# Optimization experiments

Measured on AMD Instinct MI355X. Metric: run time of the kernel, lower is better.

Reference implementation:

```python
import jax, jax.numpy as jnp
import numpy as np

EMBED = 256      # hp.embed_size
ATT = 256        # hp.attention_size
KSZ = 5          # hp.kernel_size
L = 4            # hp.decoder_layers
N_MELS = 80
R = 4
KEY_PR = (4096 // 4) / 512.0   # hp.max_frames // hp.r / hp.max_timesteps = 2.0
QUERY_PR = 1.0
SQRT_HALF = float(np.sqrt(0.5))


def _pos_enc(T, C, pos_rate):
    # Faithful to source: angle_rates = pos*pos_rate/10000^(2*(k//2)/C); pe = pos*angle_rates
    pos = jnp.arange(T, dtype=jnp.float32)[:, None]            # [T,1]
    k = jnp.arange(C)[None, :]                                  # [1,C]
    power = jnp.power(jnp.float32(10000.0), 2.0 * (k // 2).astype(jnp.float32) / C)
    angle = pos * (pos * pos_rate / power)                      # [T,C]
    return jnp.where(k % 2 == 0, jnp.sin(angle), jnp.cos(angle))[None]  # [1,T,C]


def _conv_block(x, w, b, dilation):
    # causal dilated Conv1D + GLU + scaled residual. x:[B,T,C], w:[K,C,2C]
    pad = (KSZ - 1) * dilation
    y = jax.lax.conv_general_dilated(
        x, w, window_strides=(1,), padding=[(pad, 0)], rhs_dilation=(dilation,),
        dimension_numbers=('NWC', 'WIO', 'NWC')) + b
    a, g = jnp.split(y, 2, axis=-1)
    return (x + a * jax.nn.sigmoid(g)) * SQRT_HALF


def _attention(x, keys, values, w1, b1, w2, b2, w3, b3, wo, bo):
    Tq, Tk, C = x.shape[1], keys.shape[1], x.shape[-1]
    q = x + _pos_enc(Tq, C, QUERY_PR)
    k = keys + _pos_enc(Tk, C, KEY_PR)
    k_out = k @ w1 + b1           # fc1(keys)
    q_out = q @ w2 + b2           # fc2(query)
    v_out = values @ w3 + b3      # fc3(values)
    aw = jnp.einsum('bqd,bkd->bqk', q_out, k_out)
    # key_masks = ones_like(sum(keys_out,-1)) -> never zero, masking is a no-op (kept faithful)
    al = jax.nn.softmax(aw, axis=-1)  # dropout disabled (training=False)
    ctx = jnp.einsum('bqk,bkd->bqd', al, v_out) * jax.lax.rsqrt(jnp.float32(Tk))
    return ctx @ wo + bo


def setup_inputs() -> dict:
    key = jax.random.key(0)
    ks = jax.random.split(key, 16)
    s = jnp.float32(0.02)
    B, TQ, TK = 32, 1024, 512
    d = {}
    d['inputs'] = jax.random.normal(ks[0], (B, TQ, N_MELS * R), jnp.float32)
    d['keys'] = jax.random.normal(ks[1], (B, TK, EMBED), jnp.float32)
    d['values'] = jax.random.normal(ks[2], (B, TK, EMBED), jnp.float32)
    d['w_first'] = jax.random.normal(ks[3], (N_MELS * R, EMBED), jnp.float32) * s
    d['b_first'] = jnp.zeros((EMBED,), jnp.float32)
    d['fc_w'] = jax.random.normal(ks[4], (L - 1, EMBED, EMBED), jnp.float32) * s
    d['fc_b'] = jnp.zeros((L - 1, EMBED), jnp.float32)
    d['conv_w'] = jax.random.normal(ks[5], (L, KSZ, EMBED, 2 * EMBED), jnp.float32) * s
    d['conv_b'] = jnp.zeros((L, 2 * EMBED), jnp.float32)
    d['att_w1'] = jax.random.normal(ks[6], (L, EMBED, ATT), jnp.float32) * s
    d['att_b1'] = jnp.zeros((L, ATT), jnp.float32)
    d['att_w2'] = jax.random.normal(ks[7], (L, EMBED, ATT), jnp.float32) * s
    d['att_b2'] = jnp.zeros((L, ATT), jnp.float32)
    d['att_w3'] = jax.random.normal(ks[8], (L, EMBED, ATT), jnp.float32) * s
    d['att_b3'] = jnp.zeros((L, ATT), jnp.float32)
    d['att_wo'] = jax.random.normal(ks[9], (L, ATT, EMBED), jnp.float32) * s
    d['att_bo'] = jnp.zeros((L, EMBED), jnp.float32)
    d['w_done'] = jax.random.normal(ks[10], (EMBED, 2), jnp.float32) * s
    d['b_done'] = jnp.zeros((2,), jnp.float32)
    d['w_mel'] = jax.random.normal(ks[11], (EMBED, N_MELS * R), jnp.float32) * s
    d['b_mel'] = jnp.zeros((N_MELS * R,), jnp.float32)
    return d


def reference(inputs, keys, values, w_first, b_first, fc_w, fc_b, conv_w, conv_b,
              att_w1, att_b1, att_w2, att_b2, att_w3, att_b3, att_wo, att_bo,
              w_done, b_done, w_mel, b_mel):
    h = jax.nn.relu(inputs @ w_first + b_first)
    for i in range(L - 1):
        h = jax.nn.relu(h @ fc_w[i] + fc_b[i])
    for i in range(L):
        h = _conv_block(h, conv_w[i], conv_b[i], 2 ** i)
        att = _attention(h, keys, values,
                         att_w1[i], att_b1[i], att_w2[i], att_b2[i],
                         att_w3[i], att_b3[i], att_wo[i], att_bo[i])
        h = (att + h) * SQRT_HALF
    done_output = jax.nn.sigmoid(h @ w_done + b_done)
    mel_output = h @ w_mel + b_mel
    return (mel_output, done_output, h)
```

## Files before the change

kernel.cpp:

```cpp
#include <hip/hip_runtime.h>
#include <hip/hip_bf16.h>
#include <math.h>

#define SQH 0.70710678118654752440f

typedef __bf16 bf16x8 __attribute__((ext_vector_type(8)));
typedef float f32x4 __attribute__((ext_vector_type(4)));

__device__ __forceinline__ void glds16(const void* g, void* l) {
    __builtin_amdgcn_global_load_lds((const __attribute__((address_space(1))) void*)g,
                                     (__attribute__((address_space(3))) void*)l, 16, 0, 0);
}

__device__ __forceinline__ int xcd_swz(int lin, int n) {
    if (n & 7) return lin;
    return (lin & 7) * (n >> 3) + (lin >> 3);
}

__global__ void pos_enc_kernel(float* __restrict__ pe, int T, float rate) {
    int idx = blockIdx.x * blockDim.x + threadIdx.x;
    if (idx >= T * 256) return;
    int t = idx >> 8;
    int k = idx & 255;
    float e = 2.0f * (float)(k >> 1) / 256.0f;
    float pw = powf(10000.0f, e);
    float ang = (float)t * ((float)t * rate / pw);
    pe[idx] = ((k & 1) == 0) ? sinf(ang) : cosf(ang);
}

__global__ void zero_init(float* z) { z[threadIdx.x] = 0.f; }

__global__ __launch_bounds__(256) void cvt_bf(const float* __restrict__ src,
                                              __bf16* __restrict__ dst, long n8) {
    long i = (long)blockIdx.x * 256 + threadIdx.x;
    if (i >= n8) return;
    const float* s = src + i * 8;
    float4 a = *(const float4*)s, b = *(const float4*)(s + 4);
    bf16x8 o;
    o[0] = (__bf16)a.x; o[1] = (__bf16)a.y; o[2] = (__bf16)a.z; o[3] = (__bf16)a.w;
    o[4] = (__bf16)b.x; o[5] = (__bf16)b.y; o[6] = (__bf16)b.z; o[7] = (__bf16)b.w;
    *(bf16x8*)(dst + i * 8) = o;
}

__global__ __launch_bounds__(256) void kpe_kernel(const float* __restrict__ keys,
                                                  const float* __restrict__ pek,
                                                  __bf16* __restrict__ dst) {
    long i = (long)blockIdx.x * 256 + threadIdx.x;
    long row = i >> 5; int c8 = (int)(i & 31) << 3;
    const float* kp = keys + row * 256 + c8;
    const float* pp = pek + (row & 511) * 256 + c8;
    float4 a = *(const float4*)kp, b = *(const float4*)(kp + 4);
    float4 p = *(const float4*)pp, q = *(const float4*)(pp + 4);
    bf16x8 o;
    o[0] = (__bf16)(a.x + p.x); o[1] = (__bf16)(a.y + p.y);
    o[2] = (__bf16)(a.z + p.z); o[3] = (__bf16)(a.w + p.w);
    o[4] = (__bf16)(b.x + q.x); o[5] = (__bf16)(b.y + q.y);
    o[6] = (__bf16)(b.z + q.z); o[7] = (__bf16)(b.w + q.w);
    *(bf16x8*)(dst + i * 8) = o;
}

__global__ __launch_bounds__(256) void transpose_k(const float* __restrict__ src,
                                                   __bf16* __restrict__ dst,
                                                   int R, int Cc, long sS, long sD) {
    __shared__ float tile[32][33];
    src += (long)blockIdx.z * sS;
    dst += (long)blockIdx.z * sD;
    int c0 = blockIdx.x * 32, r0 = blockIdx.y * 32;
    int tx = threadIdx.x & 31, ty = threadIdx.x >> 5;
#pragma unroll
    for (int p = 0; p < 4; ++p)
        tile[ty + 8 * p][tx] = src[(long)(r0 + ty + 8 * p) * Cc + c0 + tx];
    __syncthreads();
#pragma unroll
    for (int p = 0; p < 4; ++p)
        dst[(long)(c0 + ty + 8 * p) * R + r0 + tx] = (__bf16)tile[tx][ty + 8 * p];
}

template<int BIAS_MODE, int ACT, int OUT_MODE, int RES>
__global__ __launch_bounds__(256) void gemm_bf(
    const __bf16* __restrict__ A, const __bf16* __restrict__ Bt,
    const float* __restrict__ bias, const float* __restrict__ res,
    float* __restrict__ outF, __bf16* __restrict__ outB,
    int M, int N, int K, long sA, long sB, long sC)
{
    __shared__ __align__(16) __bf16 As[4096];
    __shared__ __align__(16) __bf16 Bs[4096];
    const int gx = gridDim.x, gy = gridDim.y;
    int lin = (blockIdx.z * gy + blockIdx.y) * gx + blockIdx.x;
    lin = xcd_swz(lin, gx * gy * gridDim.z);
    const int bx = lin % gx, by = (lin / gx) % gy, z = lin / (gx * gy);
    A += (long)z * sA;
    Bt += (long)z * sB;
    const int row0 = by << 7, col0 = bx << 7;
    const int tid = threadIdx.x, wid = tid >> 6, lane = tid & 63;
    const int lrow = lane & 15, lkp = lane >> 4;
    const int wm = (wid >> 1) << 6, wn = (wid & 1) << 6;
    const int srow = (wid << 5) + (lane >> 2);
    const int kq8 = (lane & 3) << 3;
    const __bf16* Ap0 = A + (long)(row0 + srow) * K + kq8;
    const __bf16* Ap1 = Ap0 + (long)16 * K;
    int c0i = col0 + srow, c1i = col0 + srow + 16;
    if (c0i > N - 1) c0i = N - 1;
    if (c1i > N - 1) c1i = N - 1;
    const __bf16* Bp0 = Bt + (long)c0i * K + kq8;
    const __bf16* Bp1 = Bt + (long)c1i * K + kq8;
    __bf16* AsW = As + (wid << 10);
    __bf16* BsW = Bs + (wid << 10);

    f32x4 acc[4][4];
#pragma unroll
    for (int i = 0; i < 4; ++i)
#pragma unroll
        for (int j = 0; j < 4; ++j) acc[i][j] = (f32x4){0.f, 0.f, 0.f, 0.f};

    for (int k0 = 0; k0 < K; k0 += 32) {
        glds16(Ap0 + k0, AsW);
        glds16(Ap1 + k0, AsW + 512);
        glds16(Bp0 + k0, BsW);
        glds16(Bp1 + k0, BsW + 512);
        __syncthreads();
        bf16x8 af[4], bfr[4];
        const __bf16* Ar = As + (wm + lrow) * 32 + lkp * 8;
        const __bf16* Br = Bs + (wn + lrow) * 32 + lkp * 8;
#pragma unroll
        for (int i = 0; i < 4; ++i) af[i] = *(const bf16x8*)(Ar + i * 512);
#pragma unroll
        for (int j = 0; j < 4; ++j) bfr[j] = *(const bf16x8*)(Br + j * 512);
#pragma unroll
        for (int i = 0; i < 4; ++i)
#pragma unroll
            for (int j = 0; j < 4; ++j)
                acc[i][j] = __builtin_amdgcn_mfma_f32_16x16x32_bf16(af[i], bfr[j], acc[i][j], 0, 0, 0);
        __syncthreads();
    }

    float* oF = outF ? outF + (long)z * sC : nullptr;
    __bf16* oB = outB ? outB + (long)z * sC : nullptr;
    const float* resp = RES ? res + (long)z * sC : nullptr;
#pragma unroll
    for (int i = 0; i < 4; ++i) {
#pragma unroll
        for (int r = 0; r < 4; ++r) {
            const int gr = row0 + wm + i * 16 + lkp * 4 + r;
#pragma unroll
            for (int j = 0; j < 4; ++j) {
                const int gc = col0 + wn + j * 16 + lrow;
                if (gc >= N) continue;
                float v = acc[i][j][r];
                if (BIAS_MODE == 1) v += bias[gc];
                if (BIAS_MODE == 2) v += bias[gr];
                if (RES) v = (v + resp[(long)gr * N + gc]) * SQH;
                if (ACT == 1) v = fmaxf(v, 0.f);
                if (OUT_MODE == 0 || OUT_MODE == 2) oF[(long)gr * N + gc] = v;
                if (OUT_MODE == 1 || OUT_MODE == 2) oB[(long)gr * N + gc] = (__bf16)v;
            }
        }
    }
}

__global__ __launch_bounds__(256) void conv_glu(
    const __bf16* __restrict__ hbf, const float* __restrict__ hin,
    const __bf16* __restrict__ Wt, const float* __restrict__ bias,
    const float* __restrict__ peq,
    float* __restrict__ hc_f, __bf16* __restrict__ hc_b, __bf16* __restrict__ hq_b,
    int dil, const __bf16* __restrict__ zp)
{
    __shared__ __align__(16) __bf16 As[4096];
    __shared__ __align__(16) __bf16 Ba[4096];
    __shared__ __align__(16) __bf16 Bg[4096];
    const int gx = gridDim.x;
    int lin = blockIdx.y * gx + blockIdx.x;
    lin = xcd_swz(lin, gx * gridDim.y);
    const int bx = lin % gx, by = lin / gx;
    const int row0 = by << 7, col0 = bx << 7;
    const int tid = threadIdx.x, wid = tid >> 6, lane = tid & 63;
    const int lrow = lane & 15, lkp = lane >> 4;
    const int wm = (wid >> 1) << 6, wn = (wid & 1) << 6;
    const int srow = (wid << 5) + (lane >> 2);
    const int kq8 = (lane & 3) << 3;
    const int grow = row0 + srow;
    const int t0 = (row0 & 1023) + srow;
    const __bf16* Ba0 = Wt + (long)(col0 + srow) * 1280 + kq8;
    const __bf16* Ba1 = Ba0 + (long)16 * 1280;
    const __bf16* Bg0 = Wt + (long)(col0 + 256 + srow) * 1280 + kq8;
    const __bf16* Bg1 = Bg0 + (long)16 * 1280;
    __bf16* AsW = As + (wid << 10);
    __bf16* BaW = Ba + (wid << 10);
    __bf16* BgW = Bg + (wid << 10);

    f32x4 aca[4][4], acg[4][4];
#pragma unroll
    for (int i = 0; i < 4; ++i)
#pragma unroll
        for (int j = 0; j < 4; ++j) {
            aca[i][j] = (f32x4){0.f, 0.f, 0.f, 0.f};
            acg[i][j] = (f32x4){0.f, 0.f, 0.f, 0.f};
        }

    for (int k0 = 0; k0 < 1280; k0 += 32) {
        const int tap = k0 >> 8;
        const int off = (4 - tap) * dil;
        const int kc = (k0 & 255) + kq8;
        const __bf16* a0 = (t0 >= off) ? hbf + (long)(grow - off) * 256 + kc : zp;
        const __bf16* a1 = (t0 + 16 >= off) ? hbf + (long)(grow + 16 - off) * 256 + kc : zp;
        glds16(a0, AsW);
        glds16(a1, AsW + 512);
        glds16(Ba0 + k0, BaW);
        glds16(Ba1 + k0, BaW + 512);
        glds16(Bg0 + k0, BgW);
        glds16(Bg1 + k0, BgW + 512);
        __syncthreads();
        bf16x8 af[4], ba[4], bg[4];
        const __bf16* Ar = As + (wm + lrow) * 32 + lkp * 8;
        const __bf16* Bar = Ba + (wn + lrow) * 32 + lkp * 8;
        const __bf16* Bgr = Bg + (wn + lrow) * 32 + lkp * 8;
#pragma unroll
        for (int i = 0; i < 4; ++i) af[i] = *(const bf16x8*)(Ar + i * 512);
#pragma unroll
        for (int j = 0; j < 4; ++j) { ba[j] = *(const bf16x8*)(Bar + j * 512); bg[j] = *(const bf16x8*)(Bgr + j * 512); }
#pragma unroll
        for (int i = 0; i < 4; ++i)
#pragma unroll
            for (int j = 0; j < 4; ++j) {
                aca[i][j] = __builtin_amdgcn_mfma_f32_16x16x32_bf16(af[i], ba[j], aca[i][j], 0, 0, 0);
                acg[i][j] = __builtin_amdgcn_mfma_f32_16x16x32_bf16(af[i], bg[j], acg[i][j], 0, 0, 0);
            }
        __syncthreads();
    }
#pragma unroll
    for (int i = 0; i < 4; ++i) {
#pragma unroll
        for (int r = 0; r < 4; ++r) {
            const int gr = row0 + wm + i * 16 + lkp * 4 + r;
            const long rb = (long)gr * 256;
            const long pb = (long)(gr & 1023) * 256;
#pragma unroll
            for (int j = 0; j < 4; ++j) {
                const int ca = col0 + wn + j * 16 + lrow;
                float a = aca[i][j][r] + bias[ca];
                float g = acg[i][j][r] + bias[ca + 256];
                float v = (hin[rb + ca] + a / (1.f + expf(-g))) * SQH;
                hc_f[rb + ca] = v;
                hc_b[rb + ca] = (__bf16)v;
                hq_b[rb + ca] = (__bf16)(v + peq[pb + ca]);
            }
        }
    }
}

__global__ __launch_bounds__(512) void scores_sm(
    const __bf16* __restrict__ Q, const __bf16* __restrict__ Kb,
    __bf16* __restrict__ aw)
{
    __shared__ __align__(16) __bf16 As[128 * 32];
    __shared__ __align__(16) __bf16 Bs[512 * 32];
    __shared__ float redM[4][128];
    __shared__ float redS[4][128];
    int lin = xcd_swz(blockIdx.x, gridDim.x);
    const int rt = lin & 7, z = lin >> 3;
    const int row0 = rt << 7;
    const __bf16* Az = Q + (long)z * 1024 * 256;
    const __bf16* Bz = Kb + (long)z * 512 * 256;
    __bf16* awz = aw + (long)z * 1024 * 512;
    const int tid = threadIdx.x, wid = tid >> 6, lane = tid & 63;
    const int lrow = lane & 15, lkp = lane >> 4;
    const int wr = wid >> 2, wc = wid & 3;
    const int sr = lane >> 2;
    const int kq8 = (lane & 3) << 3;

    f32x4 acc[4][8];
#pragma unroll
    for (int i = 0; i < 4; ++i)
#pragma unroll
        for (int j = 0; j < 8; ++j) acc[i][j] = (f32x4){0.f, 0.f, 0.f, 0.f};

    for (int k0 = 0; k0 < 256; k0 += 32) {
        glds16(Az + (long)(row0 + (wid << 4) + sr) * 256 + k0 + kq8, As + (wid << 9));
#pragma unroll
        for (int c = 0; c < 4; ++c) {
            const int R = ((c << 3) + wid) << 4;
            glds16(Bz + (long)(R + sr) * 256 + k0 + kq8, Bs + (R << 5));
        }
        __syncthreads();
        bf16x8 af[4], bfr[8];
        const __bf16* Ar = As + ((wr << 6) + lrow) * 32 + lkp * 8;
        const __bf16* Br = Bs + ((wc << 7) + lrow) * 32 + lkp * 8;
#pragma unroll
        for (int i = 0; i < 4; ++i) af[i] = *(const bf16x8*)(Ar + i * 512);
#pragma unroll
        for (int j = 0; j < 8; ++j) bfr[j] = *(const bf16x8*)(Br + j * 512);
#pragma unroll
        for (int i = 0; i < 4; ++i)
#pragma unroll
            for (int j = 0; j < 8; ++j)
                acc[i][j] = __builtin_amdgcn_mfma_f32_16x16x32_bf16(af[i], bfr[j], acc[i][j], 0, 0, 0);
        __syncthreads();
    }

    float mx[4][4];
#pragma unroll
    for (int i = 0; i < 4; ++i)
#pragma unroll
        for (int r = 0; r < 4; ++r) {
            float m = acc[i][0][r];
#pragma unroll
            for (int j = 1; j < 8; ++j) m = fmaxf(m, acc[i][j][r]);
#pragma unroll
            for (int s = 1; s < 16; s <<= 1) m = fmaxf(m, __shfl_xor(m, s));
            mx[i][r] = m;
        }
    if (lrow == 0) {
#pragma unroll
        for (int i = 0; i < 4; ++i)
#pragma unroll
            for (int r = 0; r < 4; ++r)
                redM[wc][(wr << 6) + i * 16 + (lkp << 2) + r] = mx[i][r];
    }
    __syncthreads();
    float sm[4][4];
#pragma unroll
    for (int i = 0; i < 4; ++i)
#pragma unroll
        for (int r = 0; r < 4; ++r) {
            const int row = (wr << 6) + i * 16 + (lkp << 2) + r;
            float m = fmaxf(fmaxf(redM[0][row], redM[1][row]), fmaxf(redM[2][row], redM[3][row]));
            float s = 0.f;
#pragma unroll
            for (int j = 0; j < 8; ++j) {
                float p = expf(acc[i][j][r] - m);
                acc[i][j][r] = p;
                s += p;
            }
#pragma unroll
            for (int sft = 1; sft < 16; sft <<= 1) s += __shfl_xor(s, sft);
            sm[i][r] = s;
        }
    if (lrow == 0) {
#pragma unroll
        for (int i = 0; i < 4; ++i)
#pragma unroll
            for (int r = 0; r < 4; ++r)
                redS[wc][(wr << 6) + i * 16 + (lkp << 2) + r] = sm[i][r];
    }
    __syncthreads();
#pragma unroll
    for (int i = 0; i < 4; ++i)
#pragma unroll
        for (int r = 0; r < 4; ++r) {
            const int row = (wr << 6) + i * 16 + (lkp << 2) + r;
            float S = redS[0][row] + redS[1][row] + redS[2][row] + redS[3][row];
            float sc = 0.04419417382415922f / S;
            __bf16* op = awz + (long)(row0 + row) * 512 + (wc << 7) + lrow;
#pragma unroll
            for (int j = 0; j < 8; ++j)
                op[j * 16] = (__bf16)(acc[i][j][r] * sc);
        }
}

__global__ __launch_bounds__(256) void done_kernel(const float* __restrict__ h,
                                                   const float* __restrict__ w,
                                                   const float* __restrict__ b,
                                                   float* __restrict__ out) {
    int row = blockIdx.x * 4 + (threadIdx.x >> 6);
    int lane = threadIdx.x & 63;
    float4 hv = *(const float4*)(h + (long)row * 256 + lane * 4);
    float4 w0 = *(const float4*)(w + lane * 8);
    float4 w1 = *(const float4*)(w + lane * 8 + 4);
    float d0 = hv.x * w0.x + hv.y * w0.z + hv.z * w1.x + hv.w * w1.z;
    float d1 = hv.x * w0.y + hv.y * w0.w + hv.z * w1.y + hv.w * w1.w;
#pragma unroll
    for (int s = 32; s; s >>= 1) { d0 += __shfl_xor(d0, s); d1 += __shfl_xor(d1, s); }
    if (lane == 0) {
        out[(long)row * 2 + 0] = 1.f / (1.f + expf(-(d0 + b[0])));
        out[(long)row * 2 + 1] = 1.f / (1.f + expf(-(d1 + b[1])));
    }
}

extern "C" void kernel_launch(void* const* d_in, const int* in_sizes, int n_in,
                              void* d_out, int out_size, void* d_ws, size_t ws_size,
                              hipStream_t stream) {
    const float* inputs  = (const float*)d_in[0];
    const float* keys    = (const float*)d_in[1];
    const float* values  = (const float*)d_in[2];
    const float* w_first = (const float*)d_in[3];
    const float* b_first = (const float*)d_in[4];
    const float* fc_w    = (const float*)d_in[5];
    const float* fc_b    = (const float*)d_in[6];
    const float* conv_w  = (const float*)d_in[7];
    const float* conv_b  = (const float*)d_in[8];
    const float* w1 = (const float*)d_in[9];  const float* b1 = (const float*)d_in[10];
    const float* w2 = (const float*)d_in[11]; const float* b2 = (const float*)d_in[12];
    const float* w3 = (const float*)d_in[13]; const float* b3 = (const float*)d_in[14];
    const float* wo = (const float*)d_in[15]; const float* bo = (const float*)d_in[16];
    const float* w_done = (const float*)d_in[17]; const float* b_done = (const float*)d_in[18];
    const float* w_mel  = (const float*)d_in[19]; const float* b_mel  = (const float*)d_in[20];
    float* out = (float*)d_out;
    float* ws  = (float*)d_ws;

    float* peq  = ws;
    float* pek  = peq + 262144;
    float* zp   = pek + 131072;
    float* h_f  = zp + 64;
    float* hc_f = h_f + 8388608;
    __bf16* h_b   = (__bf16*)(hc_f + 8388608);
    __bf16* hc_b  = h_b   + 8388608;
    __bf16* hq_b  = hc_b  + 8388608;
    __bf16* q_bf  = hq_b  + 8388608;
    __bf16* k_bf  = q_bf  + 8388608;
    __bf16* kpe_bf= k_bf  + 4194304;
    __bf16* val_bf= kpe_bf+ 4194304;
    __bf16* vT_bf = val_bf+ 4194304;
    __bf16* awb   = vT_bf + 4194304;
    __bf16* wfT   = awb   + 16777216;
    __bf16* fcT   = wfT   + 81920;
    __bf16* convT = fcT   + 196608;
    __bf16* w1T   = convT + 2621440;
    __bf16* w2T   = w1T   + 262144;
    __bf16* w3T   = w2T   + 262144;
    __bf16* woT   = w3T   + 262144;
    __bf16* wmT   = woT   + 262144;
    __bf16* in_bf = awb;
    __bf16* ctx_bf = q_bf;

    dim3 blk(256);

    pos_enc_kernel<<<1024, 256, 0, stream>>>(peq, 1024, 1.0f);
    pos_enc_kernel<<<512, 256, 0, stream>>>(pek, 512, 2.0f);
    zero_init<<<1, 64, 0, stream>>>(zp);

    cvt_bf<<<5120, 256, 0, stream>>>(inputs, in_bf, 1310720);
    cvt_bf<<<2048, 256, 0, stream>>>(values, val_bf, 524288);
    kpe_kernel<<<2048, 256, 0, stream>>>(keys, pek, kpe_bf);

    transpose_k<<<dim3(8, 10, 1), blk, 0, stream>>>(w_first, wfT, 320, 256, 0, 0);
    transpose_k<<<dim3(8, 8, 3), blk, 0, stream>>>(fc_w, fcT, 256, 256, 65536, 65536);
    transpose_k<<<dim3(16, 40, 4), blk, 0, stream>>>(conv_w, convT, 1280, 512, 655360, 655360);
    transpose_k<<<dim3(8, 8, 4), blk, 0, stream>>>(w1, w1T, 256, 256, 65536, 65536);
    transpose_k<<<dim3(8, 8, 4), blk, 0, stream>>>(w2, w2T, 256, 256, 65536, 65536);
    transpose_k<<<dim3(8, 8, 4), blk, 0, stream>>>(w3, w3T, 256, 256, 65536, 65536);
    transpose_k<<<dim3(8, 8, 4), blk, 0, stream>>>(wo, woT, 256, 256, 65536, 65536);
    transpose_k<<<dim3(10, 8, 1), blk, 0, stream>>>(w_mel, wmT, 256, 320, 0, 0);

    gemm_bf<1, 1, 1, 0><<<dim3(2, 256, 1), blk, 0, stream>>>(
        in_bf, wfT, b_first, nullptr, nullptr, h_b, 32768, 256, 320, 0, 0, 0);
    gemm_bf<1, 1, 1, 0><<<dim3(2, 256, 1), blk, 0, stream>>>(
        h_b, fcT + 0 * 65536, fc_b + 0 * 256, nullptr, nullptr, hq_b, 32768, 256, 256, 0, 0, 0);
    gemm_bf<1, 1, 1, 0><<<dim3(2, 256, 1), blk, 0, stream>>>(
        hq_b, fcT + 1 * 65536, fc_b + 1 * 256, nullptr, nullptr, hc_b, 32768, 256, 256, 0, 0, 0);
    gemm_bf<1, 1, 2, 0><<<dim3(2, 256, 1), blk, 0, stream>>>(
        hc_b, fcT + 2 * 65536, fc_b + 2 * 256, nullptr, h_f, h_b, 32768, 256, 256, 0, 0, 0);

    for (int l = 0; l < 4; ++l) {
        int dil = 1 << l;
        conv_glu<<<dim3(2, 256, 1), blk, 0, stream>>>(
            h_b, h_f, convT + (long)l * 655360, conv_b + l * 512, peq,
            hc_f, hc_b, hq_b, dil, (const __bf16*)zp);
        gemm_bf<1, 0, 1, 0><<<dim3(2, 256, 1), blk, 0, stream>>>(
            hq_b, w2T + (long)l * 65536, b2 + l * 256, nullptr, nullptr, q_bf, 32768, 256, 256, 0, 0, 0);
        gemm_bf<1, 0, 1, 0><<<dim3(2, 128, 1), blk, 0, stream>>>(
            kpe_bf, w1T + (long)l * 65536, b1 + l * 256, nullptr, nullptr, k_bf, 16384, 256, 256, 0, 0, 0);
        gemm_bf<2, 0, 1, 0><<<dim3(4, 2, 32), blk, 0, stream>>>(
            w3T + (long)l * 65536, val_bf, b3 + l * 256, nullptr, nullptr, vT_bf,
            256, 512, 256, 0, 512 * 256, 256 * 512);
        scores_sm<<<256, 512, 0, stream>>>(q_bf, k_bf, awb);
        gemm_bf<0, 0, 1, 0><<<dim3(2, 8, 32), blk, 0, stream>>>(
            awb, vT_bf, nullptr, nullptr, nullptr, ctx_bf,
            1024, 256, 512, 1024 * 512, 256 * 512, 1024 * 256);
        gemm_bf<1, 0, 2, 1><<<dim3(2, 256, 1), blk, 0, stream>>>(
            ctx_bf, woT + (long)l * 65536, bo + l * 256, hc_f, h_f, h_b, 32768, 256, 256, 0, 0, 0);
    }

    gemm_bf<1, 0, 0, 0><<<dim3(3, 256, 1), blk, 0, stream>>>(
        h_b, wmT, b_mel, nullptr, out, nullptr, 32768, 320, 256, 0, 0, 0);
    done_kernel<<<8192, 256, 0, stream>>>(h_f, w_done, b_done, out + 10485760);
    hipMemcpyAsync(out + 10551296, h_f, (size_t)8388608 * 4, hipMemcpyDeviceToDevice, stream);
}
```

Measured before the change: 1.336 ms.

## Double-buffer LDS tiles in GEMM, conv and scores kernels; narrow conv column tile

The gemm_bf, conv_glu and scores_sm kernels now use two LDS buffers. The next K-slice is issued with global_load_lds before computing on the current one, and a single vmcnt(0) wait plus barrier ends each step, so global loads overlap the MFMA work. conv_glu also shrinks its output column tile from 128 to 64, launching four column blocks instead of two, which halves its accumulator count and adds parallelism. The costs are doubled LDS use per block, which may lower occupancy, and more redundant reads of the A tile in conv.

```diff
diff --git a/kernel.cpp b/kernel.cpp
--- a/kernel.cpp
+++ b/kernel.cpp
@@ -10,6 +10,10 @@
 __device__ __forceinline__ void glds16(const void* g, void* l) {
     __builtin_amdgcn_global_load_lds((const __attribute__((address_space(1))) void*)g,
                                      (__attribute__((address_space(3))) void*)l, 16, 0, 0);
+}
+__device__ __forceinline__ void wait_vm0_barrier() {
+    asm volatile("s_waitcnt vmcnt(0)" ::: "memory");
+    __builtin_amdgcn_s_barrier();
 }
 
 __device__ __forceinline__ int xcd_swz(int lin, int n) {
@@ -83,8 +87,8 @@
     float* __restrict__ outF, __bf16* __restrict__ outB,
     int M, int N, int K, long sA, long sB, long sC)
 {
-    __shared__ __align__(16) __bf16 As[4096];
-    __shared__ __align__(16) __bf16 Bs[4096];
+    __shared__ __align__(16) __bf16 As[2][4096];
+    __shared__ __align__(16) __bf16 Bs[2][4096];
     const int gx = gridDim.x, gy = gridDim.y;
     int lin = (blockIdx.z * gy + blockIdx.y) * gx + blockIdx.x;
     lin = xcd_swz(lin, gx * gy * gridDim.z);
@@ -104,8 +108,15 @@
     if (c1i > N - 1) c1i = N - 1;
     const __bf16* Bp0 = Bt + (long)c0i * K + kq8;
     const __bf16* Bp1 = Bt + (long)c1i * K + kq8;
-    __bf16* AsW = As + (wid << 10);
-    __bf16* BsW = Bs + (wid << 10);
+
+    auto stage = [&](int b, int k0) {
+        __bf16* A_ = As[b] + (wid << 10);
+        __bf16* B_ = Bs[b] + (wid << 10);
+        glds16(Ap0 + k0, A_);
+        glds16(Ap1 + k0, A_ + 512);
+        glds16(Bp0 + k0, B_);
+        glds16(Bp1 + k0, B_ + 512);
+    };
 
     f32x4 acc[4][4];
 #pragma unroll
@@ -113,15 +124,15 @@
 #pragma unroll
         for (int j = 0; j < 4; ++j) acc[i][j] = (f32x4){0.f, 0.f, 0.f, 0.f};
 
-    for (int k0 = 0; k0 < K; k0 += 32) {
-        glds16(Ap0 + k0, AsW);
-        glds16(Ap1 + k0, AsW + 512);
-        glds16(Bp0 + k0, BsW);
-        glds16(Bp1 + k0, BsW + 512);
-        __syncthreads();
+    const int nk = K >> 5;
+    stage(0, 0);
+    wait_vm0_barrier();
+    int cur = 0;
+    for (int t = 0; t < nk; ++t) {
+        if (t + 1 < nk) stage(cur ^ 1, (t + 1) << 5);
         bf16x8 af[4], bfr[4];
-        const __bf16* Ar = As + (wm + lrow) * 32 + lkp * 8;
-        const __bf16* Br = Bs + (wn + lrow) * 32 + lkp * 8;
+        const __bf16* Ar = As[cur] + (wm + lrow) * 32 + lkp * 8;
+        const __bf16* Br = Bs[cur] + (wn + lrow) * 32 + lkp * 8;
 #pragma unroll
         for (int i = 0; i < 4; ++i) af[i] = *(const bf16x8*)(Ar + i * 512);
 #pragma unroll
@@ -131,7 +142,8 @@
 #pragma unroll
             for (int j = 0; j < 4; ++j)
                 acc[i][j] = __builtin_amdgcn_mfma_f32_16x16x32_bf16(af[i], bfr[j], acc[i][j], 0, 0, 0);
-        __syncthreads();
+        wait_vm0_barrier();
+        cur ^= 1;
     }
 
     float* oF = outF ? outF + (long)z * sC : nullptr;
@@ -165,78 +177,80 @@
     float* __restrict__ hc_f, __bf16* __restrict__ hc_b, __bf16* __restrict__ hq_b,
     int dil, const __bf16* __restrict__ zp)
 {
-    __shared__ __align__(16) __bf16 As[4096];
-    __shared__ __align__(16) __bf16 Ba[4096];
-    __shared__ __align__(16) __bf16 Bg[4096];
+    __shared__ __align__(16) __bf16 As[2][4096];
+    __shared__ __align__(16) __bf16 Bas[2][2048];
+    __shared__ __align__(16) __bf16 Bgs[2][2048];
     const int gx = gridDim.x;
     int lin = blockIdx.y * gx + blockIdx.x;
     lin = xcd_swz(lin, gx * gridDim.y);
     const int bx = lin % gx, by = lin / gx;
-    const int row0 = by << 7, col0 = bx << 7;
+    const int row0 = by << 7, col0 = bx << 6;
     const int tid = threadIdx.x, wid = tid >> 6, lane = tid & 63;
     const int lrow = lane & 15, lkp = lane >> 4;
-    const int wm = (wid >> 1) << 6, wn = (wid & 1) << 6;
-    const int srow = (wid << 5) + (lane >> 2);
+    const int wr = wid >> 1, wc = wid & 1;
+    const int sA = (wid << 5) + (lane >> 2);
     const int kq8 = (lane & 3) << 3;
-    const int grow = row0 + srow;
-    const int t0 = (row0 & 1023) + srow;
-    const __bf16* Ba0 = Wt + (long)(col0 + srow) * 1280 + kq8;
-    const __bf16* Ba1 = Ba0 + (long)16 * 1280;
-    const __bf16* Bg0 = Wt + (long)(col0 + 256 + srow) * 1280 + kq8;
-    const __bf16* Bg1 = Bg0 + (long)16 * 1280;
-    __bf16* AsW = As + (wid << 10);
-    __bf16* BaW = Ba + (wid << 10);
-    __bf16* BgW = Bg + (wid << 10);
-
-    f32x4 aca[4][4], acg[4][4];
-#pragma unroll
-    for (int i = 0; i < 4; ++i)
-#pragma unroll
-        for (int j = 0; j < 4; ++j) {
-            aca[i][j] = (f32x4){0.f, 0.f, 0.f, 0.f};
-            acg[i][j] = (f32x4){0.f, 0.f, 0.f, 0.f};
-        }
-
-    for (int k0 = 0; k0 < 1280; k0 += 32) {
+    const int grow = row0 + sA;
+    const int t0 = (row0 & 1023) + sA;
+    const int cB = col0 + (wid << 4) + (lane >> 2);
+    const __bf16* Ba0 = Wt + (long)cB * 1280 + kq8;
+    const __bf16* Bg0 = Wt + (long)(cB + 256) * 1280 + kq8;
+
+    auto stage = [&](int b, int k0) {
         const int tap = k0 >> 8;
         const int off = (4 - tap) * dil;
         const int kc = (k0 & 255) + kq8;
         const __bf16* a0 = (t0 >= off) ? hbf + (long)(grow - off) * 256 + kc : zp;
         const __bf16* a1 = (t0 + 16 >= off) ? hbf + (long)(grow + 16 - off) * 256 + kc : zp;
-        glds16(a0, AsW);
-        glds16(a1, AsW + 512);
-        glds16(Ba0 + k0, BaW);
-        glds16(Ba1 + k0, BaW + 512);
-        glds16(Bg0 + k0, BgW);
-        glds16(Bg1 + k0, BgW + 512);
-        __syncthreads();
-        bf16x8 af[4], ba[4], bg[4];
-        const __bf16* Ar = As + (wm + lrow) * 32 + lkp * 8;
-        const __bf16* Bar = Ba + (wn + lrow) * 32 + lkp * 8;
-        const __bf16* Bgr = Bg + (wn + lrow) * 32 + lkp * 8;
+        __bf16* A_ = As[b] + (wid << 10);
+        glds16(a0, A_);
+        glds16(a1, A_ + 512);
+        glds16(Ba0 + k0, Bas[b] + (wid << 9));
+        glds16(Bg0 + k0, Bgs[b] + (wid << 9));
+    };
+
+    f32x4 aca[4][2], acg[4][2];
+#pragma unroll
+    for (int i = 0; i < 4; ++i)
+#pragma unroll
+        for (int j = 0; j < 2; ++j) {
+            aca[i][j] = (f32x4){0.f, 0.f, 0.f, 0.f};
+            acg[i][j] = (f32x4){0.f, 0.f, 0.f, 0.f};
+        }
+
+    stage(0, 0);
+    wait_vm0_barrier();
+    int cur = 0;
+    for (int t = 0; t < 40; ++t) {
+        if (t + 1 < 40) stage(cur ^ 1, (t + 1) << 5);
+        bf16x8 af[4], ba[2], bg[2];
+        const __bf16* Ar = As[cur] + ((wr << 6) + lrow) * 32 + lkp * 8;
+        const __bf16* Bar = Bas[cur] + ((wc << 5) + lrow) * 32 + lkp * 8;
+        const __bf16* Bgr = Bgs[cur] + ((wc << 5) + lrow) * 32 + lkp * 8;
 #pragma unroll
         for (int i = 0; i < 4; ++i) af[i] = *(const bf16x8*)(Ar + i * 512);
 #pragma unroll
-        for (int j = 0; j < 4; ++j) { ba[j] = *(const bf16x8*)(Bar + j * 512); bg[j] = *(const bf16x8*)(Bgr + j * 512); }
+        for (int j = 0; j < 2; ++j) { ba[j] = *(const bf16x8*)(Bar + j * 512); bg[j] = *(const bf16x8*)(Bgr + j * 512); }
 #pragma unroll
         for (int i = 0; i < 4; ++i)
 #pragma unroll
-            for (int j = 0; j < 4; ++j) {
+            for (int j = 0; j < 2; ++j) {
                 aca[i][j] = __builtin_amdgcn_mfma_f32_16x16x32_bf16(af[i], ba[j], aca[i][j], 0, 0, 0);
                 acg[i][j] = __builtin_amdgcn_mfma_f32_16x16x32_bf16(af[i], bg[j], acg[i][j], 0, 0, 0);
             }
-        __syncthreads();
+        wait_vm0_barrier();
+        cur ^= 1;
     }
 #pragma unroll
     for (int i = 0; i < 4; ++i) {
 #pragma unroll
         for (int r = 0; r < 4; ++r) {
-            const int gr = row0 + wm + i * 16 + lkp * 4 + r;
+            const int gr = row0 + (wr << 6) + i * 16 + lkp * 4 + r;
             const long rb = (long)gr * 256;
             const long pb = (long)(gr & 1023) * 256;
 #pragma unroll
-            for (int j = 0; j < 4; ++j) {
-                const int ca = col0 + wn + j * 16 + lrow;
+            for (int j = 0; j < 2; ++j) {
+                const int ca = col0 + (wc << 5) + j * 16 + lrow;
                 float a = aca[i][j][r] + bias[ca];
                 float g = acg[i][j][r] + bias[ca + 256];
                 float v = (hin[rb + ca] + a / (1.f + expf(-g))) * SQH;
@@ -252,8 +266,8 @@
     const __bf16* __restrict__ Q, const __bf16* __restrict__ Kb,
     __bf16* __restrict__ aw)
 {
-    __shared__ __align__(16) __bf16 As[128 * 32];
-    __shared__ __align__(16) __bf16 Bs[512 * 32];
+    __shared__ __align__(16) __bf16 As[2][128 * 32];
+    __shared__ __align__(16) __bf16 Bs[2][512 * 32];
     __shared__ float redM[4][128];
     __shared__ float redS[4][128];
     int lin = xcd_swz(blockIdx.x, gridDim.x);
@@ -268,23 +282,29 @@
     const int sr = lane >> 2;
     const int kq8 = (lane & 3) << 3;
 
-    f32x4 acc[4][8];
-#pragma unroll
-    for (int i = 0; i < 4; ++i)
-#pragma unroll
-        for (int j = 0; j < 8; ++j) acc[i][j] = (f32x4){0.f, 0.f, 0.f, 0.f};
-
-    for (int k0 = 0; k0 < 256; k0 += 32) {
-        glds16(Az + (long)(row0 + (wid << 4) + sr) * 256 + k0 + kq8, As + (wid << 9));
+    auto stage = [&](int b, int k0) {
+        glds16(Az + (long)(row0 + (wid << 4) + sr) * 256 + k0 + kq8, As[b] + (wid << 9));
 #pragma unroll
         for (int c = 0; c < 4; ++c) {
             const int R = ((c << 3) + wid) << 4;
-            glds16(Bz + (long)(R + sr) * 256 + k0 + kq8, Bs + (R << 5));
-        }
-        __syncthreads();
+            glds16(Bz + (long)(R + sr) * 256 + k0 + kq8, Bs[b] + (R << 5));
+        }
+    };
+
+    f32x4 acc[4][8];
+#pragma unroll
+    for (int i = 0; i < 4; ++i)
+#pragma unroll
+        for (int j = 0; j < 8; ++j) acc[i][j] = (f32x4){0.f, 0.f, 0.f, 0.f};
+
+    stage(0, 0);
+    wait_vm0_barrier();
+    int cur = 0;
+    for (int t = 0; t < 8; ++t) {
+        if (t + 1 < 8) stage(cur ^ 1, (t + 1) << 5);
         bf16x8 af[4], bfr[8];
-        const __bf16* Ar = As + ((wr << 6) + lrow) * 32 + lkp * 8;
-        const __bf16* Br = Bs + ((wc << 7) + lrow) * 32 + lkp * 8;
+        const __bf16* Ar = As[cur] + ((wr << 6) + lrow) * 32 + lkp * 8;
+        const __bf16* Br = Bs[cur] + ((wc << 7) + lrow) * 32 + lkp * 8;
 #pragma unroll
         for (int i = 0; i < 4; ++i) af[i] = *(const bf16x8*)(Ar + i * 512);
 #pragma unroll
@@ -294,7 +314,8 @@
 #pragma unroll
             for (int j = 0; j < 8; ++j)
                 acc[i][j] = __builtin_amdgcn_mfma_f32_16x16x32_bf16(af[i], bfr[j], acc[i][j], 0, 0, 0);
-        __syncthreads();
+        wait_vm0_barrier();
+        cur ^= 1;
     }
 
     float mx[4][4];
@@ -452,7 +473,7 @@
 
     for (int l = 0; l < 4; ++l) {
         int dil = 1 << l;
-        conv_glu<<<dim3(2, 256, 1), blk, 0, stream>>>(
+        conv_glu<<<dim3(4, 256, 1), blk, 0, stream>>>(
             h_b, h_f, convT + (long)l * 655360, conv_b + l * 512, peq,
             hc_f, hc_b, hq_b, dil, (const __bf16*)zp);
         gemm_bf<1, 0, 1, 0><<<dim3(2, 256, 1), blk, 0, stream>>>(
```

After: 1.236 ms. 1.08x faster.
